# Performance work log

Measured on AMD Instinct MI355X. Metric: run time of the kernel, lower is better.

## Reference

```python
import jax, jax.numpy as jnp
import numpy as np

N, E, H, D_IN, D_OUT, DEPTH, G = 100000, 1600000, 128, 128, 10, 3, 256


def setup_inputs() -> dict:
    key = jax.random.key(0)
    ks = jax.random.split(key, 16)
    s = lambda k, shape: jax.random.normal(k, shape, dtype=jnp.float32) * 0.05
    inp = {
        "x": jax.random.normal(ks[0], (N, D_IN), dtype=jnp.float32),
        "edge_index": jax.random.randint(ks[1], (2, E), 0, N, dtype=jnp.int32),
        "control_edge_index": jax.random.randint(ks[2], (2, 1024), 0, N, dtype=jnp.int32),
        "batch": jnp.sort(jax.random.randint(ks[3], (N,), 0, G, dtype=jnp.int32)),
        # encoder MLP: input_dim -> hidden -> hidden
        "enc_w1": s(ks[4], (D_IN, H)), "enc_b1": jnp.zeros((H,), jnp.float32),
        "enc_w2": s(ks[5], (H, H)),    "enc_b2": jnp.zeros((H,), jnp.float32),
        # conv_depth GCN layers, hidden -> hidden
        "conv_w": s(ks[6], (DEPTH, H, H)), "conv_b": jnp.zeros((DEPTH, H), jnp.float32),
        # decoder MLP: hidden -> hidden -> output_dim
        "dec_w1": s(ks[7], (H, H)),     "dec_b1": jnp.zeros((H,), jnp.float32),
        "dec_w2": s(ks[8], (H, D_OUT)), "dec_b2": jnp.zeros((D_OUT,), jnp.float32),
    }
    return inp


def _gcn_forward(x, enc_w1, enc_b1, enc_w2, enc_b2, conv_w, conv_b,
                 dec_w1, dec_b1, dec_w2, dec_b2, edge_index, batch):
    # encoder MLP (Linear-ReLU-Dropout(eval)-Linear)
    h = jax.nn.relu(x @ enc_w1 + enc_b1) @ enc_w2 + enc_b2

    # GCN normalization with self-loops: D^{-1/2} (A + I) D^{-1/2}
    loops = jnp.arange(N, dtype=edge_index.dtype)
    src = jnp.concatenate([edge_index[0], loops])  # [E + N]
    dst = jnp.concatenate([edge_index[1], loops])
    deg = jax.ops.segment_sum(jnp.ones_like(src, dtype=h.dtype), dst, num_segments=N)
    inv_sqrt = jax.lax.rsqrt(deg)  # deg >= 1 thanks to self-loops
    coef = (inv_sqrt[src] * inv_sqrt[dst])[:, None]  # [E+N, 1]

    for l in range(DEPTH):
        hw = h @ conv_w[l] + conv_b[l]                      # [N, H]
        h = jax.ops.segment_sum(hw[src] * coef, dst, num_segments=N)
        if l < DEPTH - 1:  # linear=False -> nonlinearity between convs
            h = jax.nn.relu(h)

    # global_add_pool over graph ids
    pooled = jax.ops.segment_sum(h, batch, num_segments=G)   # [G, H]

    # decoder MLP
    return jax.nn.relu(pooled @ dec_w1 + dec_b1) @ dec_w2 + dec_b2  # [G, D_OUT]


def reference(x, edge_index, control_edge_index, batch, enc_w1, enc_b1, enc_w2,
              enc_b2, conv_w, conv_b, dec_w1, dec_b1, dec_w2, dec_b2):
    # control_edge_index corresponds to the (disabled) control mechanism; unused
    return _gcn_forward(x, enc_w1, enc_b1, enc_w2, enc_b2, conv_w, conv_b,
                        dec_w1, dec_b1, dec_w2, dec_b2, edge_index, batch)
```

## Files before the change

### kernel.cpp

```cpp
#include <hip/hip_runtime.h>
#include <hip/hip_bf16.h>
#include <cstdint>
#include <cstddef>

#define NN 100000
#define NE 1600000
#define HH 128
#define NG 256

#define NB 196
#define BSH 9
#define BMSK 511
#define CHUNK 16384
#define NBLK 98

typedef __bf16 bf16x8 __attribute__((ext_vector_type(8)));
typedef float floatx4 __attribute__((ext_vector_type(4)));

__device__ __forceinline__ uint32_t f2b(float f) {
  union { float f; uint32_t u; } v; v.f = f;
  uint32_t u = v.u;
  return (u + 0x7FFFu + ((u >> 16) & 1u)) >> 16;
}
__device__ __forceinline__ float b2f(uint32_t h) {
  union { uint32_t u; float f; } v; v.u = h << 16;
  return v.f;
}
__device__ __forceinline__ void addrow(float* a, uint4 v) {
  a[0] += b2f(v.x & 0xFFFFu); a[1] += b2f(v.x >> 16);
  a[2] += b2f(v.y & 0xFFFFu); a[3] += b2f(v.y >> 16);
  a[4] += b2f(v.z & 0xFFFFu); a[5] += b2f(v.z >> 16);
  a[6] += b2f(v.w & 0xFFFFu); a[7] += b2f(v.w >> 16);
}


__global__ __launch_bounds__(256) void k_cntA(const int* __restrict__ src,
                                              int* __restrict__ blkcnt) {
  __shared__ int h[NB];
  int t = threadIdx.x;
  if (t < NB) h[t] = 0;
  __syncthreads();
  int base = blockIdx.x * CHUNK, end = min(base + CHUNK, NE);
  for (int i = base + t; i < end; i += 256) atomicAdd(&h[src[i] >> BSH], 1);
  __syncthreads();
  if (t < NB) blkcnt[blockIdx.x * NB + t] = h[t];
}

__global__ __launch_bounds__(256) void k_cntB(const uint2* __restrict__ pairs,
                                              int* __restrict__ blkcnt) {
  __shared__ int h[NB];
  int t = threadIdx.x;
  if (t < NB) h[t] = 0;
  __syncthreads();
  int base = blockIdx.x * CHUNK, end = min(base + CHUNK, NE);
  for (int i = base + t; i < end; i += 256) atomicAdd(&h[pairs[i].y >> BSH], 1);
  __syncthreads();
  if (t < NB) blkcnt[blockIdx.x * NB + t] = h[t];
}

__global__ __launch_bounds__(64) void k_colscan(const int* __restrict__ blkcnt,
                                                int* __restrict__ poff,
                                                int* __restrict__ colsum) {
  int b = blockIdx.x, t = threadIdx.x;
  int carry = 0;
  for (int base = 0; base < NBLK; base += 64) {
    int r = base + t;
    int x = (r < NBLK) ? blkcnt[r * NB + b] : 0;
    int v = x;
    for (int d = 1; d < 64; d <<= 1) { int u = __shfl_up(v, d); if (t >= d) v += u; }
    if (r < NBLK) poff[r * NB + b] = carry + v - x;
    carry += __shfl(v, 63);
  }
  if (t == 0) colsum[b] = carry;
}

__global__ void k_gscan(const int* __restrict__ colsum, int* __restrict__ gbase,
                        int* __restrict__ off, int set_off) {
  __shared__ int s[256];
  int t = threadIdx.x;
  int x = (t < NB) ? colsum[t] : 0;
  s[t] = x; __syncthreads();
  for (int d = 1; d < 256; d <<= 1) {
    int v = (t >= d) ? s[t - d] : 0;
    __syncthreads();
    s[t] += v;
    __syncthreads();
  }
  if (t < NB) gbase[t] = s[t] - x;
  if (t == 0) { gbase[NB] = NE; if (set_off) off[NN] = NE; }
}

__global__ __launch_bounds__(256) void k_placeA(const int* __restrict__ src,
                                                const int* __restrict__ dst,
                                                const int* __restrict__ poff,
                                                const int* __restrict__ gbase,
                                                uint2* __restrict__ pairs) {
  __shared__ int cur[NB];
  int t = threadIdx.x;
  if (t < NB) cur[t] = poff[blockIdx.x * NB + t] + gbase[t];
  __syncthreads();
  int base = blockIdx.x * CHUNK, end = min(base + CHUNK, NE);
  for (int i = base + t; i < end; i += 256) {
    int s = src[i], d = dst[i];
    int p = atomicAdd(&cur[s >> BSH], 1);
    pairs[p] = make_uint2((unsigned)s, (unsigned)d);
  }
}

__global__ __launch_bounds__(256) void k_placeB(const uint2* __restrict__ pairs,
                                                const int* __restrict__ poff,
                                                const int* __restrict__ gbase,
                                                uint32_t* __restrict__ outb) {
  __shared__ int cur[NB];
  int t = threadIdx.x;
  if (t < NB) cur[t] = poff[blockIdx.x * NB + t] + gbase[t];
  __syncthreads();
  int base = blockIdx.x * CHUNK, end = min(base + CHUNK, NE);
  for (int i = base + t; i < end; i += 256) {
    uint2 v = pairs[i];
    int p = atomicAdd(&cur[v.y >> BSH], 1);
    outb[p] = v.x | ((v.y & (unsigned)BMSK) << 17);
  }
}

__global__ __launch_bounds__(256) void k_bucket_sort(
    const uint32_t* __restrict__ pairbuf, const int* __restrict__ gbase,
    int* __restrict__ off, float* __restrict__ inv, int* __restrict__ csrs)
{
  __shared__ int cnt[512];
  __shared__ int loff[512];
  __shared__ int psum[256];
  int b = blockIdx.x;
  int tid = threadIdx.x;
  cnt[tid] = 0; cnt[tid + 256] = 0;
  __syncthreads();
  int s0 = gbase[b], s1 = gbase[b + 1];
  for (int i = s0 + tid; i < s1; i += 256)
    atomicAdd(&cnt[pairbuf[i] >> 17], 1);
  __syncthreads();
  int a0 = cnt[2 * tid], a1 = cnt[2 * tid + 1];
  int s = a0 + a1;
  psum[tid] = s;
  __syncthreads();
  for (int d = 1; d < 256; d <<= 1) {
    int v = (tid >= d) ? psum[tid - d] : 0;
    __syncthreads();
    psum[tid] += v;
    __syncthreads();
  }
  int excl = psum[tid] - s;
  loff[2 * tid] = excl;
  loff[2 * tid + 1] = excl + a0;
  __syncthreads();
#pragma unroll
  for (int k = 0; k < 2; ++k) {
    int i = tid + k * 256;
    int node = b * 512 + i;
    if (node < NN) {
      off[node] = s0 + loff[i];
      inv[node] = rsqrtf((float)cnt[i] + 1.0f);
    }
  }
  __syncthreads();
  cnt[tid] = loff[tid]; cnt[tid + 256] = loff[tid + 256];
  __syncthreads();
  for (int i = s0 + tid; i < s1; i += 256) {
    uint32_t v = pairbuf[i];
    int p = atomicAdd(&cnt[v >> 17], 1);
    csrs[s0 + p] = (int)(v & 0x1FFFFu);
  }
}

__global__ __launch_bounds__(256) void k_nodeprep(const int* __restrict__ off,
                                                  const int* __restrict__ batch,
                                                  int* __restrict__ dhist,
                                                  int* __restrict__ gstart) {
  __shared__ int h[64];
  int t = threadIdx.x;
  if (t < 64) h[t] = 0;
  __syncthreads();
  int i = blockIdx.x * 256 + t;
  if (i < NN) {
    int d = off[i + 1] - off[i]; if (d > 63) d = 63;
    atomicAdd(&h[d], 1);
    int b = batch[i];
    if (i == 0) {
      for (int g = 0; g <= b; ++g) gstart[g] = 0;
    } else {
      int a = batch[i - 1];
      for (int g = a + 1; g <= b; ++g) gstart[g] = i;
    }
    if (i == NN - 1) {
      for (int g = b + 1; g <= NG; ++g) gstart[g] = NN;
    }
  }
  __syncthreads();
  if (t < 64 && h[t]) atomicAdd(&dhist[t], h[t]);
}

__global__ void k_dscan(const int* __restrict__ dhist, int* __restrict__ dcur) {
  int t = threadIdx.x;
  int x = dhist[63 - t];
  int v = x;
  for (int d = 1; d < 64; d <<= 1) { int u = __shfl_up(v, d); if (t >= d) v += u; }
  dcur[63 - t] = v - x;
}

__global__ __launch_bounds__(256) void k_dplace(const int* __restrict__ off,
                                                int* __restrict__ dcur,
                                                int* __restrict__ order) {
  __shared__ int h[64], base[64];
  int t = threadIdx.x;
  if (t < 64) h[t] = 0;
  __syncthreads();
  int i = blockIdx.x * 256 + t;
  int d = 0, ld = 0;
  if (i < NN) { d = off[i + 1] - off[i]; if (d > 63) d = 63; ld = atomicAdd(&h[d], 1); }
  __syncthreads();
  if (t < 64) base[t] = h[t] ? atomicAdd(&dcur[t], h[t]) : 0;
  __syncthreads();
  if (i < NN) order[base[d] + ld] = i;
}

__global__ __launch_bounds__(256) void k_gemm(
    const uint16_t* __restrict__ A16, const float* __restrict__ A32,
    const float* __restrict__ W, const float* __restrict__ bias,
    const float* __restrict__ scale,
    uint16_t* __restrict__ Out, int M, int do_relu)
{
  __shared__ uint16_t Wt[128][136];
  const int tid = threadIdx.x;

  for (int it = 0; it < 16; ++it) {
    int idx = tid + it * 256;
    int n = idx & 127;
    int k0 = (idx >> 7) * 4;
    uint2 wv;
    wv.x = f2b(W[(k0 + 0) * 128 + n]) | (f2b(W[(k0 + 1) * 128 + n]) << 16);
    wv.y = f2b(W[(k0 + 2) * 128 + n]) | (f2b(W[(k0 + 3) * 128 + n]) << 16);
    *(uint2*)&Wt[n][k0] = wv;
  }
  __syncthreads();

  const int lane = tid & 63;
  const int wave = tid >> 6;
  const int lrow = lane & 15;
  const int lk = (lane >> 4) * 8;
  const int row0 = blockIdx.x * 128 + wave * 32;

  floatx4 acc[2][8];
#pragma unroll
  for (int t = 0; t < 2; ++t)
#pragma unroll
    for (int n = 0; n < 8; ++n)
      acc[t][n] = (floatx4){0.f, 0.f, 0.f, 0.f};

#pragma unroll
  for (int ks = 0; ks < 4; ++ks) {
    bf16x8 a[2];
#pragma unroll
    for (int t = 0; t < 2; ++t) {
      int r = row0 + t * 16 + lrow;
      uint4 tmp = {0u, 0u, 0u, 0u};
      if (r < M) {
        if (A32) {
          float4 f0 = *(const float4*)(A32 + (size_t)r * HH + ks * 32 + lk);
          float4 f1 = *(const float4*)(A32 + (size_t)r * HH + ks * 32 + lk + 4);
          tmp.x = f2b(f0.x) | (f2b(f0.y) << 16);
          tmp.y = f2b(f0.z) | (f2b(f0.w) << 16);
          tmp.z = f2b(f1.x) | (f2b(f1.y) << 16);
          tmp.w = f2b(f1.z) | (f2b(f1.w) << 16);
        } else {
          tmp = *(const uint4*)(A16 + (size_t)r * HH + ks * 32 + lk);
        }
      }
      a[t] = __builtin_bit_cast(bf16x8, tmp);
    }
#pragma unroll
    for (int n = 0; n < 8; ++n) {
      bf16x8 b = __builtin_bit_cast(bf16x8, *(const uint4*)&Wt[n * 16 + lrow][ks * 32 + lk]);
      acc[0][n] = __builtin_amdgcn_mfma_f32_16x16x32_bf16(a[0], b, acc[0][n], 0, 0, 0);
      acc[1][n] = __builtin_amdgcn_mfma_f32_16x16x32_bf16(a[1], b, acc[1][n], 0, 0, 0);
    }
  }

  float bc[8];
#pragma unroll
  for (int n = 0; n < 8; ++n) bc[n] = bias[n * 16 + lrow];

  const int rbase = (lane >> 4) * 4;
#pragma unroll
  for (int t = 0; t < 2; ++t) {
#pragma unroll
    for (int r = 0; r < 4; ++r) {
      int row = row0 + t * 16 + rbase + r;
      if (row < M) {
        float sc = scale ? scale[row] : 1.0f;
#pragma unroll
        for (int n = 0; n < 8; ++n) {
          float v = acc[t][n][r] + bc[n];
          if (do_relu) v = fmaxf(v, 0.f);
          v *= sc;
          Out[(size_t)row * HH + n * 16 + lrow] = (uint16_t)f2b(v);
        }
      }
    }
  }
}

__global__ __launch_bounds__(256) void k_agg(
    const uint16_t* __restrict__ hw2, const int* __restrict__ off,
    const int* __restrict__ csrs, const float* __restrict__ inv,
    const int* __restrict__ order,
    uint16_t* __restrict__ hout, int do_relu)
{
  int slot = blockIdx.x * 16 + (threadIdx.x >> 4);
  if (slot >= NN) return;
  int node = order[slot];
  int c = (threadIdx.x & 15) * 8;

  uint4 sv = *(const uint4*)(hw2 + (size_t)node * HH + c);
  float a[8] = {0.f, 0.f, 0.f, 0.f, 0.f, 0.f, 0.f, 0.f};
  addrow(a, sv);

  int e0 = off[node], e1 = off[node + 1];
  int e = e0;
  for (; e + 4 <= e1; e += 4) {
    int s0 = csrs[e + 0], s1 = csrs[e + 1], s2 = csrs[e + 2], s3 = csrs[e + 3];
    uint4 v0 = *(const uint4*)(hw2 + (size_t)s0 * HH + c);
    uint4 v1 = *(const uint4*)(hw2 + (size_t)s1 * HH + c);
    uint4 v2 = *(const uint4*)(hw2 + (size_t)s2 * HH + c);
    uint4 v3 = *(const uint4*)(hw2 + (size_t)s3 * HH + c);
    addrow(a, v0); addrow(a, v1); addrow(a, v2); addrow(a, v3);
  }
  for (; e < e1; ++e) {
    int s = csrs[e];
    uint4 v = *(const uint4*)(hw2 + (size_t)s * HH + c);
    addrow(a, v);
  }
  float invd = inv[node];
#pragma unroll
  for (int j = 0; j < 8; ++j) {
    a[j] *= invd;
    if (do_relu) a[j] = fmaxf(a[j], 0.f);
  }
  uint4 o;
  o.x = f2b(a[0]) | (f2b(a[1]) << 16);
  o.y = f2b(a[2]) | (f2b(a[3]) << 16);
  o.z = f2b(a[4]) | (f2b(a[5]) << 16);
  o.w = f2b(a[6]) | (f2b(a[7]) << 16);
  *(uint4*)(hout + (size_t)node * HH + c) = o;
}

__global__ __launch_bounds__(256) void k_pool(const uint16_t* __restrict__ h,
                                              const int* __restrict__ gstart,
                                              float* __restrict__ pooled) {
  __shared__ float red[16][132];
  int g = blockIdx.x;
  int tid = threadIdx.x;
  int slot = tid >> 4;
  int c = (tid & 15) * 8;

  int r0 = gstart[g], r1 = gstart[g + 1];
  float a[8] = {0.f, 0.f, 0.f, 0.f, 0.f, 0.f, 0.f, 0.f};
  for (int r = r0 + slot; r < r1; r += 16) {
    uint4 v = *(const uint4*)(h + (size_t)r * HH + c);
    a[0] += b2f(v.x & 0xFFFFu); a[1] += b2f(v.x >> 16);
    a[2] += b2f(v.y & 0xFFFFu); a[3] += b2f(v.y >> 16);
    a[4] += b2f(v.z & 0xFFFFu); a[5] += b2f(v.z >> 16);
    a[6] += b2f(v.w & 0xFFFFu); a[7] += b2f(v.w >> 16);
  }
  *(float4*)&red[slot][c]     = make_float4(a[0], a[1], a[2], a[3]);
  *(float4*)&red[slot][c + 4] = make_float4(a[4], a[5], a[6], a[7]);
  __syncthreads();
  if (tid < 128) {
    float s = 0.f;
#pragma unroll
    for (int k = 0; k < 16; ++k) s += red[k][tid];
    pooled[g * HH + tid] = s;
  }
}

__global__ void k_dec(const float* __restrict__ pooled,
                      const float* __restrict__ w1, const float* __restrict__ b1,
                      const float* __restrict__ w2, const float* __restrict__ b2,
                      float* __restrict__ out) {
  __shared__ float p[128], t[128];
  int g = blockIdx.x, j = threadIdx.x;
  p[j] = pooled[g * HH + j];
  __syncthreads();
  float a = b1[j];
  for (int k = 0; k < 128; ++k) a += p[k] * w1[k * 128 + j];
  t[j] = fmaxf(a, 0.f);
  __syncthreads();
  if (j < 10) {
    float o = b2[j];
    for (int k = 0; k < 128; ++k) o += t[k] * w2[k * 10 + j];
    out[g * 10 + j] = o;
  }
}

extern "C" void kernel_launch(void* const* d_in, const int* in_sizes, int n_in,
                              void* d_out, int out_size, void* d_ws, size_t ws_size,
                              hipStream_t stream) {
  const float* x       = (const float*)d_in[0];
  const int*   eidx    = (const int*)d_in[1];
  const int*   src     = eidx;
  const int*   dst     = eidx + NE;
  const int*   batch   = (const int*)d_in[3];
  const float* enc_w1  = (const float*)d_in[4];
  const float* enc_b1  = (const float*)d_in[5];
  const float* enc_w2  = (const float*)d_in[6];
  const float* enc_b2  = (const float*)d_in[7];
  const float* conv_w  = (const float*)d_in[8];
  const float* conv_b  = (const float*)d_in[9];
  const float* dec_w1  = (const float*)d_in[10];
  const float* dec_b1  = (const float*)d_in[11];
  const float* dec_w2  = (const float*)d_in[12];
  const float* dec_b2  = (const float*)d_in[13];
  float* out = (float*)d_out;

  char* ws = (char*)d_ws;
  size_t o = 0;
  auto alloc = [&](size_t bytes) -> char* {
    char* p = ws + o;
    o += (bytes + 255) & ~(size_t)255;
    return p;
  };
  int*      off     = (int*)alloc((size_t)(NN + 1) * 4);
  int*      csrs    = (int*)alloc((size_t)NE * 4);
  float*    inv     = (float*)alloc((size_t)NN * 4);
  float*    pooled  = (float*)alloc((size_t)NG * HH * 4);
  int*      blkcntA = (int*)alloc((size_t)NBLK * NB * 4);
  int*      poffA   = (int*)alloc((size_t)NBLK * NB * 4);
  int*      blkcntB = (int*)alloc((size_t)NBLK * NB * 4);
  int*      poffB   = (int*)alloc((size_t)NBLK * NB * 4);
  int*      colsumA = (int*)alloc((size_t)NB * 4);
  int*      colsumB = (int*)alloc((size_t)NB * 4);
  int*      gbaseA  = (int*)alloc((size_t)(NB + 1) * 4);
  int*      gbaseB  = (int*)alloc((size_t)(NB + 1) * 4);
  int*      dhist   = (int*)alloc(64 * 4);
  int*      dcur    = (int*)alloc(64 * 4);
  int*      order   = (int*)alloc((size_t)NN * 4);
  int*      gstart  = (int*)alloc((size_t)(NG + 1) * 4);
  uint16_t* buf0    = (uint16_t*)alloc((size_t)NN * HH * 2);
  uint16_t* buf1    = (uint16_t*)alloc((size_t)NN * HH * 2);
  uint2*    pairsA  = (uint2*)buf1;
  uint32_t* pairB   = (uint32_t*)((char*)buf1 + (size_t)NE * 8);

  hipMemsetAsync(dhist, 0, 64 * 4, stream);

  k_cntA<<<dim3(NBLK), dim3(256), 0, stream>>>(src, blkcntA);
  k_colscan<<<dim3(NB), dim3(64), 0, stream>>>(blkcntA, poffA, colsumA);
  k_gscan<<<dim3(1), dim3(256), 0, stream>>>(colsumA, gbaseA, off, 0);
  k_placeA<<<dim3(NBLK), dim3(256), 0, stream>>>(src, dst, poffA, gbaseA, pairsA);
  k_cntB<<<dim3(NBLK), dim3(256), 0, stream>>>(pairsA, blkcntB);
  k_colscan<<<dim3(NB), dim3(64), 0, stream>>>(blkcntB, poffB, colsumB);
  k_gscan<<<dim3(1), dim3(256), 0, stream>>>(colsumB, gbaseB, off, 1);
  k_placeB<<<dim3(NBLK), dim3(256), 0, stream>>>(pairsA, poffB, gbaseB, pairB);
  k_bucket_sort<<<dim3(NB), dim3(256), 0, stream>>>(pairB, gbaseB, off, inv, csrs);

  const int NBK = (NN + 255) / 256;
  k_nodeprep<<<dim3(NBK), dim3(256), 0, stream>>>(off, batch, dhist, gstart);
  k_dscan<<<dim3(1), dim3(64), 0, stream>>>(dhist, dcur);
  k_dplace<<<dim3(NBK), dim3(256), 0, stream>>>(off, dcur, order);

  const int GB = (NN + 127) / 128;
  k_gemm<<<dim3(GB), dim3(256), 0, stream>>>(nullptr, x, enc_w1, enc_b1, nullptr, buf1, NN, 1);
  k_gemm<<<dim3(GB), dim3(256), 0, stream>>>(buf1, nullptr, enc_w2, enc_b2, nullptr, buf0, NN, 0);

  const int AB = (NN + 15) / 16;
  k_gemm<<<dim3(GB), dim3(256), 0, stream>>>(buf0, nullptr, conv_w + 0 * 16384, conv_b + 0,   inv, buf1, NN, 0);
  k_agg <<<dim3(AB), dim3(256), 0, stream>>>(buf1, off, csrs, inv, order, buf0, 1);
  k_gemm<<<dim3(GB), dim3(256), 0, stream>>>(buf0, nullptr, conv_w + 1 * 16384, conv_b + 128, inv, buf1, NN, 0);
  k_agg <<<dim3(AB), dim3(256), 0, stream>>>(buf1, off, csrs, inv, order, buf0, 1);
  k_gemm<<<dim3(GB), dim3(256), 0, stream>>>(buf0, nullptr, conv_w + 2 * 16384, conv_b + 256, inv, buf1, NN, 0);
  k_agg <<<dim3(AB), dim3(256), 0, stream>>>(buf1, off, csrs, inv, order, buf0, 0);

  k_pool<<<dim3(NG), dim3(256), 0, stream>>>(buf0, gstart, pooled);
  k_dec<<<dim3(NG), dim3(128), 0, stream>>>(pooled, dec_w1, dec_b1, dec_w2, dec_b2, out);
}
```

Before: 523.9 us.

## Fuse node prep into bucket sort, stage GEMM stores via LDS, fuse pool+decoder

Moves the degree histogram and graph-start computation into the bucket-sort kernel, using per-block histograms that k_dscan reduces, so the separate nodeprep kernel and memset go away. The GEMM epilogue now writes results into shared memory and then emits coalesced 16-byte row stores instead of scattered 2-byte stores. Pooling and the decoder MLP are merged into one kernel. Together these cut launch count and uncoalesced global writes, at the cost of extra barriers and reuse of the weight LDS buffer in the GEMM.

Result: slower. 544.6 us (+3.9%).

```diff
diff --git a/kernel.cpp b/kernel.cpp
--- a/kernel.cpp
+++ b/kernel.cpp
@@ -125,7 +125,9 @@
 
 __global__ __launch_bounds__(256) void k_bucket_sort(
     const uint32_t* __restrict__ pairbuf, const int* __restrict__ gbase,
-    int* __restrict__ off, float* __restrict__ inv, int* __restrict__ csrs)
+    const int* __restrict__ batch,
+    int* __restrict__ off, float* __restrict__ inv, int* __restrict__ csrs,
+    int* __restrict__ dhist2, int* __restrict__ gstart)
 {
   __shared__ int cnt[512];
   __shared__ int loff[512];
@@ -152,6 +154,9 @@
   loff[2 * tid] = excl;
   loff[2 * tid + 1] = excl + a0;
   __syncthreads();
+  int* h64 = psum;
+  if (tid < 64) h64[tid] = 0;
+  __syncthreads();
 #pragma unroll
   for (int k = 0; k < 2; ++k) {
     int i = tid + k * 256;
@@ -159,9 +164,21 @@
     if (node < NN) {
       off[node] = s0 + loff[i];
       inv[node] = rsqrtf((float)cnt[i] + 1.0f);
-    }
-  }
-  __syncthreads();
+      int d = cnt[i]; if (d > 63) d = 63;
+      atomicAdd(&h64[d], 1);
+    }
+  }
+  {
+    int n0 = b * 512, n1 = min(n0 + 512, NN);
+    for (int i = n0 + tid; i < n1; i += 256) {
+      int bb = batch[i];
+      if (i == 0) { for (int g = 0; g <= bb; ++g) gstart[g] = 0; }
+      else { int aa = batch[i - 1]; for (int g = aa + 1; g <= bb; ++g) gstart[g] = i; }
+      if (i == NN - 1) { for (int g = bb + 1; g <= NG; ++g) gstart[g] = NN; }
+    }
+  }
+  __syncthreads();
+  if (tid < 64) dhist2[b * 64 + tid] = h64[tid];
   cnt[tid] = loff[tid]; cnt[tid + 256] = loff[tid + 256];
   __syncthreads();
   for (int i = s0 + tid; i < s1; i += 256) {
@@ -171,39 +188,13 @@
   }
 }
 
-__global__ __launch_bounds__(256) void k_nodeprep(const int* __restrict__ off,
-                                                  const int* __restrict__ batch,
-                                                  int* __restrict__ dhist,
-                                                  int* __restrict__ gstart) {
-  __shared__ int h[64];
-  int t = threadIdx.x;
-  if (t < 64) h[t] = 0;
-  __syncthreads();
-  int i = blockIdx.x * 256 + t;
-  if (i < NN) {
-    int d = off[i + 1] - off[i]; if (d > 63) d = 63;
-    atomicAdd(&h[d], 1);
-    int b = batch[i];
-    if (i == 0) {
-      for (int g = 0; g <= b; ++g) gstart[g] = 0;
-    } else {
-      int a = batch[i - 1];
-      for (int g = a + 1; g <= b; ++g) gstart[g] = i;
-    }
-    if (i == NN - 1) {
-      for (int g = b + 1; g <= NG; ++g) gstart[g] = NN;
-    }
-  }
-  __syncthreads();
-  if (t < 64 && h[t]) atomicAdd(&dhist[t], h[t]);
-}
-
-__global__ void k_dscan(const int* __restrict__ dhist, int* __restrict__ dcur) {
-  int t = threadIdx.x;
-  int x = dhist[63 - t];
-  int v = x;
+__global__ void k_dscan(const int* __restrict__ dhist2, int* __restrict__ dcur) {
+  int t = threadIdx.x;
+  int sum = 0;
+  for (int r = 0; r < NB; ++r) sum += dhist2[r * 64 + (63 - t)];
+  int v = sum;
   for (int d = 1; d < 64; d <<= 1) { int u = __shfl_up(v, d); if (t >= d) v += u; }
-  dcur[63 - t] = v - x;
+  dcur[63 - t] = v - sum;
 }
 
 __global__ __launch_bounds__(256) void k_dplace(const int* __restrict__ off,
@@ -288,23 +279,36 @@
 #pragma unroll
   for (int n = 0; n < 8; ++n) bc[n] = bias[n * 16 + lrow];
 
+  __syncthreads();
+  uint16_t* tbuf = ((uint16_t*)Wt) + wave * (16 * 136);
   const int rbase = (lane >> 4) * 4;
+  const int trow = lane >> 2;
+  const int tseg = (lane & 3) * 32;
+
 #pragma unroll
   for (int t = 0; t < 2; ++t) {
 #pragma unroll
     for (int r = 0; r < 4; ++r) {
-      int row = row0 + t * 16 + rbase + r;
-      if (row < M) {
-        float sc = scale ? scale[row] : 1.0f;
-#pragma unroll
-        for (int n = 0; n < 8; ++n) {
-          float v = acc[t][n][r] + bc[n];
-          if (do_relu) v = fmaxf(v, 0.f);
-          v *= sc;
-          Out[(size_t)row * HH + n * 16 + lrow] = (uint16_t)f2b(v);
-        }
+      int grow = row0 + t * 16 + rbase + r;
+      float sc = (scale && grow < M) ? scale[grow] : 1.0f;
+#pragma unroll
+      for (int n = 0; n < 8; ++n) {
+        float v = acc[t][n][r] + bc[n];
+        if (do_relu) v = fmaxf(v, 0.f);
+        v *= sc;
+        tbuf[(rbase + r) * 136 + n * 16 + lrow] = (uint16_t)f2b(v);
       }
     }
+    __syncthreads();
+    int grow = row0 + t * 16 + trow;
+    if (grow < M) {
+#pragma unroll
+      for (int j = 0; j < 4; ++j) {
+        uint4 v = *(const uint4*)&tbuf[trow * 136 + tseg + j * 8];
+        *(uint4*)(Out + (size_t)grow * HH + tseg + j * 8) = v;
+      }
+    }
+    __syncthreads();
   }
 }
 
@@ -352,10 +356,14 @@
   *(uint4*)(hout + (size_t)node * HH + c) = o;
 }
 
-__global__ __launch_bounds__(256) void k_pool(const uint16_t* __restrict__ h,
-                                              const int* __restrict__ gstart,
-                                              float* __restrict__ pooled) {
+__global__ __launch_bounds__(256) void k_pooldec(
+    const uint16_t* __restrict__ h, const int* __restrict__ gstart,
+    const float* __restrict__ w1, const float* __restrict__ b1,
+    const float* __restrict__ w2, const float* __restrict__ b2,
+    float* __restrict__ out)
+{
   __shared__ float red[16][132];
+  __shared__ float p[128], tmpv[128];
   int g = blockIdx.x;
   int tid = threadIdx.x;
   int slot = tid >> 4;
@@ -377,26 +385,19 @@
     float s = 0.f;
 #pragma unroll
     for (int k = 0; k < 16; ++k) s += red[k][tid];
-    pooled[g * HH + tid] = s;
-  }
-}
-
-__global__ void k_dec(const float* __restrict__ pooled,
-                      const float* __restrict__ w1, const float* __restrict__ b1,
-                      const float* __restrict__ w2, const float* __restrict__ b2,
-                      float* __restrict__ out) {
-  __shared__ float p[128], t[128];
-  int g = blockIdx.x, j = threadIdx.x;
-  p[j] = pooled[g * HH + j];
-  __syncthreads();
-  float a = b1[j];
-  for (int k = 0; k < 128; ++k) a += p[k] * w1[k * 128 + j];
-  t[j] = fmaxf(a, 0.f);
-  __syncthreads();
-  if (j < 10) {
-    float o = b2[j];
-    for (int k = 0; k < 128; ++k) o += t[k] * w2[k * 10 + j];
-    out[g * 10 + j] = o;
+    p[tid] = s;
+  }
+  __syncthreads();
+  if (tid < 128) {
+    float acc1 = b1[tid];
+    for (int k = 0; k < 128; ++k) acc1 += p[k] * w1[k * 128 + tid];
+    tmpv[tid] = fmaxf(acc1, 0.f);
+  }
+  __syncthreads();
+  if (tid < 10) {
+    float o = b2[tid];
+    for (int k = 0; k < 128; ++k) o += tmpv[k] * w2[k * 10 + tid];
+    out[g * 10 + tid] = o;
   }
 }
 
@@ -430,7 +431,6 @@
   int*      off     = (int*)alloc((size_t)(NN + 1) * 4);
   int*      csrs    = (int*)alloc((size_t)NE * 4);
   float*    inv     = (float*)alloc((size_t)NN * 4);
-  float*    pooled  = (float*)alloc((size_t)NG * HH * 4);
   int*      blkcntA = (int*)alloc((size_t)NBLK * NB * 4);
   int*      poffA   = (int*)alloc((size_t)NBLK * NB * 4);
   int*      blkcntB = (int*)alloc((size_t)NBLK * NB * 4);
@@ -439,7 +439,7 @@
   int*      colsumB = (int*)alloc((size_t)NB * 4);
   int*      gbaseA  = (int*)alloc((size_t)(NB + 1) * 4);
   int*      gbaseB  = (int*)alloc((size_t)(NB + 1) * 4);
-  int*      dhist   = (int*)alloc(64 * 4);
+  int*      dhist2  = (int*)alloc((size_t)NB * 64 * 4);
   int*      dcur    = (int*)alloc(64 * 4);
   int*      order   = (int*)alloc((size_t)NN * 4);
   int*      gstart  = (int*)alloc((size_t)(NG + 1) * 4);
@@ -447,8 +447,6 @@
   uint16_t* buf1    = (uint16_t*)alloc((size_t)NN * HH * 2);
   uint2*    pairsA  = (uint2*)buf1;
   uint32_t* pairB   = (uint32_t*)((char*)buf1 + (size_t)NE * 8);
-
-  hipMemsetAsync(dhist, 0, 64 * 4, stream);
 
   k_cntA<<<dim3(NBLK), dim3(256), 0, stream>>>(src, blkcntA);
   k_colscan<<<dim3(NB), dim3(64), 0, stream>>>(blkcntA, poffA, colsumA);
@@ -458,11 +456,11 @@
   k_colscan<<<dim3(NB), dim3(64), 0, stream>>>(blkcntB, poffB, colsumB);
   k_gscan<<<dim3(1), dim3(256), 0, stream>>>(colsumB, gbaseB, off, 1);
   k_placeB<<<dim3(NBLK), dim3(256), 0, stream>>>(pairsA, poffB, gbaseB, pairB);
-  k_bucket_sort<<<dim3(NB), dim3(256), 0, stream>>>(pairB, gbaseB, off, inv, csrs);
+  k_bucket_sort<<<dim3(NB), dim3(256), 0, stream>>>(pairB, gbaseB, batch, off, inv, csrs,
+                                                    dhist2, gstart);
 
   const int NBK = (NN + 255) / 256;
-  k_nodeprep<<<dim3(NBK), dim3(256), 0, stream>>>(off, batch, dhist, gstart);
-  k_dscan<<<dim3(1), dim3(64), 0, stream>>>(dhist, dcur);
+  k_dscan<<<dim3(1), dim3(64), 0, stream>>>(dhist2, dcur);
   k_dplace<<<dim3(NBK), dim3(256), 0, stream>>>(off, dcur, order);
 
   const int GB = (NN + 127) / 128;
@@ -477,6 +475,5 @@
   k_gemm<<<dim3(GB), dim3(256), 0, stream>>>(buf0, nullptr, conv_w + 2 * 16384, conv_b + 256, inv, buf1, NN, 0);
   k_agg <<<dim3(AB), dim3(256), 0, stream>>>(buf1, off, csrs, inv, order, buf0, 0);
 
-  k_pool<<<dim3(NG), dim3(256), 0, stream>>>(buf0, gstart, pooled);
-  k_dec<<<dim3(NG), dim3(128), 0, stream>>>(pooled, dec_w1, dec_b1, dec_w2, dec_b2, out);
-}
+  k_pooldec<<<dim3(NG), dim3(256), 0, stream>>>(buf0, gstart, dec_w1, dec_b1, dec_w2, dec_b2, out);
+}
```
